# Optimization experiments

Hardware: AMD Instinct MI355X
Metric: run time of the kernel (lower is better)

## Reference

```python
import jax, jax.numpy as jnp
import numpy as np

BN_EPS = 1e-5

def _bn(h, gamma, beta):
    # training-mode BatchNorm1d over node dim, biased variance (as torch)
    m = jnp.mean(h, axis=0)
    v = jnp.var(h, axis=0)
    return (h - m) * jax.lax.rsqrt(v + BN_EPS) * gamma + beta

def _gin(x, edge_index, W, b, n_nodes):
    # PyG GINConv (eps=0): h = Linear(x + sum_{j in N(i)} x_j)
    src, dst = edge_index[0], edge_index[1]
    agg = jax.ops.segment_sum(x[src], dst, num_segments=n_nodes)
    return (x + agg) @ W + b

def setup_inputs() -> dict:
    key = jax.random.key(0)
    ks = jax.random.split(key, 16)
    N, E, D, H, G = 50000, 800000, 128, 256, 64
    x = jax.random.normal(ks[0], (N, D), dtype=jnp.float32)
    edge_index = jax.random.randint(ks[1], (2, E), 0, N, dtype=jnp.int64)
    batch = jnp.sort(jax.random.randint(ks[2], (N,), 0, G, dtype=jnp.int64))
    s = 0.05
    return {
        "x": x, "edge_index": edge_index, "batch": batch, "num_graphs": G,
        "W1": jax.random.normal(ks[3], (D, H), jnp.float32) * s,
        "b1": jnp.zeros((H,), jnp.float32),
        "W2": jax.random.normal(ks[4], (H, H), jnp.float32) * s,
        "b2": jnp.zeros((H,), jnp.float32),
        "W3": jax.random.normal(ks[5], (H, H), jnp.float32) * s,
        "b3": jnp.zeros((H,), jnp.float32),
        "g1": jnp.ones((H,), jnp.float32), "be1": jnp.zeros((H,), jnp.float32),
        "g2": jnp.ones((H,), jnp.float32), "be2": jnp.zeros((H,), jnp.float32),
        "g3": jnp.ones((H,), jnp.float32), "be3": jnp.zeros((H,), jnp.float32),
        "fcW1": jax.random.normal(ks[6], (H, H), jnp.float32) * s,
        "fcb1": jnp.zeros((H,), jnp.float32),
        "fcW2": jax.random.normal(ks[7], (H, 1), jnp.float32) * s,
        "fcb2": jnp.zeros((1,), jnp.float32),
    }

def reference(x, edge_index, batch, num_graphs, W1, b1, W2, b2, W3, b3,
              g1, be1, g2, be2, g3, be3, fcW1, fcb1, fcW2, fcb2):
    n_nodes = x.shape[0]
    # dropout treated as identity (eval / deterministic)
    x1 = jax.nn.relu(_bn(_gin(x, edge_index, W1, b1, n_nodes), g1, be1))
    x2 = jax.nn.relu(_bn(_gin(x1, edge_index, W2, b2, n_nodes), g2, be2)) + x1
    x3 = jax.nn.relu(_bn(_gin(x2, edge_index, W3, b3, n_nodes), g3, be3)) + x2
    # global mean pool over graphs
    sums = jax.ops.segment_sum(x3, batch, num_segments=num_graphs)
    cnt = jax.ops.segment_sum(jnp.ones((n_nodes,), x3.dtype), batch, num_segments=num_graphs)
    pooled = sums / jnp.maximum(cnt, 1.0)[:, None]
    h = jax.nn.relu(pooled @ fcW1 + fcb1)
    return h @ fcW2 + fcb2
```

## Files before the change

kernel.cpp:

```cpp
#include <hip/hip_runtime.h>
#include <hip/hip_bf16.h>
#include <stdint.h>

#define HDIM 256
#define NGRAPH 64

typedef short s16x8 __attribute__((ext_vector_type(8)));
typedef float f32x4 __attribute__((ext_vector_type(4)));

__device__ __forceinline__ float bf2f(unsigned short u){
    union { unsigned int i; float f; } x; x.i = ((unsigned int)u) << 16; return x.f;
}
__device__ __forceinline__ unsigned short f2bf(float f){
    union { float f; unsigned int i; } x; x.f = f;
    unsigned int r = x.i + 0x7fffu + ((x.i >> 16) & 1u);
    return (unsigned short)(r >> 16);
}
__device__ __forceinline__ float ldf(const void* p, int i, int f32){
    return f32 ? ((const float*)p)[i] : bf2f(((const unsigned short*)p)[i]);
}

__global__ void detect_kernel(const unsigned short* __restrict__ x,
                              const int* __restrict__ ei, const int* __restrict__ batch,
                              int E, int N, int* __restrict__ flags){
    if (threadIdx.x == 0 && blockIdx.x == 0){
        int c = 0;
        for (int i = 0; i < 128; i++){
            unsigned e = (x[2 * i] >> 7) & 0xFFu;
            if (e >= 100u && e <= 140u) c++;
        }
        flags[0] = (c < 96) ? 1 : 0;
        int z = (ei[2*E - 1] == 0) && (ei[2*E - 3] == 0) && (ei[2*E - 5] == 0) && (ei[2*E - 7] == 0);
        flags[1] = z ? 1 : 0;
        flags[2] = (batch[N - 1] == 0) ? 1 : 0;
    }
}

__global__ void zero_kernel(int* __restrict__ p, int n){
    int i = blockIdx.x * 256 + threadIdx.x;
    if (i < n) p[i] = 0;
}

__global__ void cvt_kernel(const void* __restrict__ src, unsigned short* __restrict__ dst,
                           int n8, const int* __restrict__ flags){
    int i = blockIdx.x * 256 + threadIdx.x;
    if (i >= n8) return;
    int base = i * 8;
    int f32 = flags[0];
    unsigned short o[8];
    if (f32){
        const float* s = (const float*)src + base;
        float4 a = *(const float4*)s;
        float4 b = *(const float4*)(s + 4);
        o[0]=f2bf(a.x); o[1]=f2bf(a.y); o[2]=f2bf(a.z); o[3]=f2bf(a.w);
        o[4]=f2bf(b.x); o[5]=f2bf(b.y); o[6]=f2bf(b.z); o[7]=f2bf(b.w);
    } else {
        *(uint4*)o = *(const uint4*)((const unsigned short*)src + base);
    }
    *(uint4*)&dst[base] = *(uint4*)o;
}

__global__ void hist_kernel(const int* __restrict__ ei, int E, int N,
                            const int* __restrict__ flags, int* __restrict__ deg){
    int e = blockIdx.x * 256 + threadIdx.x;
    if (e < E){
        int is64 = flags[1];
        int d = is64 ? ei[2 * E + 2 * e] : ei[E + e];
        if ((unsigned)d < (unsigned)N) atomicAdd(&deg[d], 1);
    }
}

__global__ void scan1_kernel(const int* __restrict__ deg, int N,
                             int* __restrict__ incl, int* __restrict__ bsums){
    __shared__ int sm[256];
    int t = threadIdx.x;
    int i = blockIdx.x * 256 + t;
    int v = (i < N) ? deg[i] : 0;
    sm[t] = v; __syncthreads();
    for (int off = 1; off < 256; off <<= 1){
        int tv = (t >= off) ? sm[t - off] : 0;
        __syncthreads();
        sm[t] += tv;
        __syncthreads();
    }
    if (i < N) incl[i] = sm[t];
    if (t == 255) bsums[blockIdx.x] = sm[255];
}

__global__ void scan23_kernel(const int* __restrict__ deg, int N, int E, int nb,
                              const int* __restrict__ bsums, int* __restrict__ rowptr){
    __shared__ int sm[256];
    int t = threadIdx.x;
    int bid = blockIdx.x;
    sm[t] = (t < nb && t < bid) ? bsums[t] : 0;
    __syncthreads();
    for (int s = 128; s > 0; s >>= 1){
        if (t < s) sm[t] += sm[t + s];
        __syncthreads();
    }
    int prefix = sm[0];
    int i = bid * 256 + t;
    if (i < N) rowptr[i] = rowptr[i] - deg[i] + prefix;
    if (i == 0) rowptr[N] = E;
}

__global__ void fill_kernel(const int* __restrict__ ei, int E, int N,
                            const int* __restrict__ flags,
                            const int* __restrict__ rowptr, int* __restrict__ fillc,
                            int* __restrict__ csr){
    int e = blockIdx.x * 256 + threadIdx.x;
    if (e < E){
        int is64 = flags[1];
        int d = is64 ? ei[2 * E + 2 * e] : ei[E + e];
        int s = is64 ? ei[2 * e]         : ei[e];
        if ((unsigned)d < (unsigned)N){
            int p = atomicAdd(&fillc[d], 1);
            csr[rowptr[d] + p] = s;
        }
    }
}

__global__ void transpose3_kernel(const void* __restrict__ W1, unsigned short* __restrict__ Wt1,
                                  const void* __restrict__ W2, unsigned short* __restrict__ Wt2,
                                  const void* __restrict__ W3, unsigned short* __restrict__ Wt3,
                                  const int* __restrict__ flags){
    int f32 = flags[0];
    int bid = blockIdx.x;
    const void* W; unsigned short* Wt; int K, base;
    if (bid < 128)      { W = W1; Wt = Wt1; K = 128; base = bid; }
    else if (bid < 384) { W = W2; Wt = Wt2; K = 256; base = bid - 128; }
    else                { W = W3; Wt = Wt3; K = 256; base = bid - 384; }
    int idx = base * 256 + threadIdx.x;
    int n = idx / K, k = idx - n * K;
    Wt[idx] = f2bf(ldf(W, k * 256 + n, f32));
}

template<int C>
__global__ __launch_bounds__(256) void agg_vec(const unsigned short* __restrict__ feat, int ldi,
                                               const int* __restrict__ rowptr, const int* __restrict__ csr,
                                               unsigned short* __restrict__ Y, int ldo, int N){
    constexpr int L   = C / 8;
    constexpr int NPB = 256 / L;
    int node = blockIdx.x * NPB + threadIdx.x / L;
    int lane = threadIdx.x & (L - 1);
    if (node >= N) return;
    int c0 = lane * 8;
    const unsigned short* base = feat + c0;

    unsigned short t0[8];
    *(uint4*)t0 = *(const uint4*)&feat[(size_t)node * ldi + c0];
    float acc[8];
    #pragma unroll
    for (int j = 0; j < 8; j++) acc[j] = bf2f(t0[j]);

    int lo = rowptr[node], hi = rowptr[node + 1];
    int e = lo;
    for (; e + 3 < hi; e += 4){
        int s0 = csr[e], s1 = csr[e + 1], s2 = csr[e + 2], s3 = csr[e + 3];
        unsigned short ta[8], tb[8], tc[8], td[8];
        *(uint4*)ta = *(const uint4*)&base[(size_t)s0 * ldi];
        *(uint4*)tb = *(const uint4*)&base[(size_t)s1 * ldi];
        *(uint4*)tc = *(const uint4*)&base[(size_t)s2 * ldi];
        *(uint4*)td = *(const uint4*)&base[(size_t)s3 * ldi];
        #pragma unroll
        for (int j = 0; j < 8; j++)
            acc[j] += (bf2f(ta[j]) + bf2f(tb[j])) + (bf2f(tc[j]) + bf2f(td[j]));
    }
    for (; e < hi; e++){
        int s0 = csr[e];
        unsigned short ta[8];
        *(uint4*)ta = *(const uint4*)&base[(size_t)s0 * ldi];
        #pragma unroll
        for (int j = 0; j < 8; j++) acc[j] += bf2f(ta[j]);
    }
    unsigned short o[8];
    #pragma unroll
    for (int j = 0; j < 8; j++) o[j] = f2bf(acc[j]);
    *(uint4*)&Y[(size_t)node * ldo + c0] = *(uint4*)o;
}

__global__ __launch_bounds__(256) void gemm_tile(
    unsigned short* __restrict__ AC, int K,
    const unsigned short* __restrict__ Bt, const void* __restrict__ bias,
    int M, const int* __restrict__ flags,
    float* __restrict__ S, float* __restrict__ Q)
{
    __shared__ __align__(16) unsigned short As[64 * 40];
    __shared__ __align__(16) unsigned short Bs[256 * 40];
    __shared__ float sS[256], sQ[256];
    const int tid  = threadIdx.x;
    const int wave = tid >> 6, lane = tid & 63;
    const int quad = lane >> 4, l16 = lane & 15;
    const int m0   = blockIdx.x * 64;
    const int wn   = wave * 64;
    const bool full = (m0 + 64 <= M);
    const int f32  = flags[0];

    sS[tid] = 0.f; sQ[tid] = 0.f;

    const f32x4 zero4 = {0.f, 0.f, 0.f, 0.f};
    f32x4 acc[4][4];
    #pragma unroll
    for (int i = 0; i < 4; i++)
        #pragma unroll
        for (int j = 0; j < 4; j++) acc[i][j] = zero4;

    for (int kc = 0; kc < K; kc += 32){
        {
            int r = tid >> 2, cc = (tid & 3) * 8;
            int gr = m0 + r;
            uint4 va; va.x = va.y = va.z = va.w = 0u;
            if (full || gr < M) va = *(const uint4*)&AC[(size_t)gr * HDIM + kc + cc];
            *(uint4*)&As[r * 40 + cc] = va;
        }
        #pragma unroll
        for (int j = 0; j < 4; j++){
            int c = tid + j * 256;
            int n = c >> 2, cc = (c & 3) * 8;
            *(uint4*)&Bs[n * 40 + cc] = *(const uint4*)&Bt[(size_t)n * K + kc + cc];
        }
        __syncthreads();
        s16x8 af[4], bfr[4];
        #pragma unroll
        for (int mt = 0; mt < 4; mt++)
            af[mt] = *(const s16x8*)&As[(mt * 16 + l16) * 40 + quad * 8];
        #pragma unroll
        for (int nt = 0; nt < 4; nt++)
            bfr[nt] = *(const s16x8*)&Bs[(wn + nt * 16 + l16) * 40 + quad * 8];
        #pragma unroll
        for (int mt = 0; mt < 4; mt++)
            #pragma unroll
            for (int nt = 0; nt < 4; nt++)
                acc[mt][nt] = __builtin_amdgcn_mfma_f32_16x16x32_bf16(af[mt], bfr[nt], acc[mt][nt], 0, 0, 0);
        __syncthreads();
    }
    #pragma unroll
    for (int nt = 0; nt < 4; nt++){
        int gc = wn + nt * 16 + l16;
        float bv = ldf(bias, gc, f32);
        float ps = 0.f, pq = 0.f;
        #pragma unroll
        for (int mt = 0; mt < 4; mt++){
            #pragma unroll
            for (int r = 0; r < 4; r++){
                int gr = m0 + mt * 16 + quad * 4 + r;
                if (full || gr < M){
                    float val = acc[mt][nt][r] + bv;
                    AC[(size_t)gr * HDIM + gc] = f2bf(val);
                    ps += val; pq += val * val;
                }
            }
        }
        atomicAdd(&sS[gc], ps);
        atomicAdd(&sQ[gc], pq);
    }
    __syncthreads();
    atomicAdd(&S[tid], sS[tid]);
    atomicAdd(&Q[tid], sQ[tid]);
}

__global__ void bnrelu_kernel(const unsigned short* __restrict__ Hin,
                              const float* __restrict__ S, const float* __restrict__ Q,
                              const void* __restrict__ g, const void* __restrict__ be,
                              float invM, const int* __restrict__ flags,
                              const unsigned short* __restrict__ res,
                              unsigned short* __restrict__ Out, int total16){
    __shared__ float sscale[256], sshift[256];
    int tid = threadIdx.x;
    {
        int f32 = flags[0];
        float m  = S[tid] * invM;
        float v  = Q[tid] * invM - m * m;
        float sc = ldf(g, tid, f32) * rsqrtf(v + 1e-5f);
        sscale[tid] = sc;
        sshift[tid] = ldf(be, tid, f32) - m * sc;
    }
    __syncthreads();
    int idx = blockIdx.x * 256 + tid;
    if (idx >= total16) return;
    #pragma unroll
    for (int h = 0; h < 2; h++){
        int base = idx * 16 + h * 8;
        int c = base & (HDIM - 1);
        unsigned short hv[8], rv[8], ov[8];
        *(uint4*)hv = *(const uint4*)&Hin[base];
        if (res) *(uint4*)rv = *(const uint4*)&res[base];
        #pragma unroll
        for (int j = 0; j < 8; j++){
            float v = bf2f(hv[j]) * sscale[c + j] + sshift[c + j];
            v = (v < 0.f) ? 0.f : v;
            if (res) v += bf2f(rv[j]);
            ov[j] = f2bf(v);
        }
        *(uint4*)&Out[base] = *(uint4*)ov;
    }
}

__global__ __launch_bounds__(256) void bnrelu_pool_kernel(
    const unsigned short* __restrict__ H, const unsigned short* __restrict__ res,
    const float* __restrict__ S, const float* __restrict__ Q,
    const void* __restrict__ g, const void* __restrict__ be,
    float invM, const int* __restrict__ flags,
    const int* __restrict__ batch, int N, float* __restrict__ sums)
{
    int r0 = blockIdx.x * 128;
    if (r0 >= N) return;
    int r1 = min(r0 + 128, N);
    int t = threadIdx.x;
    int f32 = flags[0];
    float m  = S[t] * invM;
    float v  = Q[t] * invM - m * m;
    float sc = ldf(g, t, f32) * rsqrtf(v + 1e-5f);
    float sh = ldf(be, t, f32) - m * sc;
    int stride = flags[2] ? 2 : 1;
    float acc = 0.f;
    int curg = batch[r0 * stride];
    for (int r = r0; r < r1; r++){
        int gg = batch[r * stride];
        if (gg != curg){
            atomicAdd(&sums[curg * HDIM + t], acc);
            acc = 0.f; curg = gg;
        }
        float hv = bf2f(H[(size_t)r * HDIM + t]) * sc + sh;
        hv = (hv < 0.f) ? 0.f : hv;
        hv += bf2f(res[(size_t)r * HDIM + t]);
        acc += hv;
    }
    atomicAdd(&sums[curg * HDIM + t], acc);
}

__global__ __launch_bounds__(256) void head_kernel(const float* __restrict__ sums,
                                                   const int* __restrict__ batch, int N,
                                                   const void* __restrict__ fcW1,
                                                   const void* __restrict__ fcb1,
                                                   const void* __restrict__ fcW2,
                                                   const void* __restrict__ fcb2,
                                                   void* __restrict__ out,
                                                   const int* __restrict__ flags){
    __shared__ float sp[256];
    __shared__ float red[256];
    __shared__ int scnt;
    int g = blockIdx.x, j = threadIdx.x;
    int f32 = flags[0];
    int stride = flags[2] ? 2 : 1;
    if (j == 0){
        int lo = 0, hi = N;
        while (lo < hi){ int mid = (lo + hi) >> 1; if (batch[mid * stride] < g) lo = mid + 1; else hi = mid; }
        int a = lo;
        lo = 0; hi = N;
        while (lo < hi){ int mid = (lo + hi) >> 1; if (batch[mid * stride] < g + 1) lo = mid + 1; else hi = mid; }
        scnt = lo - a;
    }
    __syncthreads();
    sp[j] = sums[g * HDIM + j] / (float)max(scnt, 1);
    __syncthreads();
    float acc = ldf(fcb1, j, f32);
    for (int k = 0; k < HDIM; k++) acc += sp[k] * ldf(fcW1, k * HDIM + j, f32);
    acc = (acc < 0.f) ? 0.f : acc;
    red[j] = acc * ldf(fcW2, j, f32);
    __syncthreads();
    for (int s = 128; s > 0; s >>= 1){
        if (j < s) red[j] += red[j + s];
        __syncthreads();
    }
    if (j == 0){
        float r = red[0] + ldf(fcb2, 0, f32);
        if (f32) ((float*)out)[g] = r;
        else     ((unsigned short*)out)[g] = f2bf(r);
    }
}

extern "C" void kernel_launch(void* const* d_in, const int* in_sizes, int n_in,
                              void* d_out, int out_size, void* d_ws, size_t ws_size,
                              hipStream_t stream)
{
    const unsigned short* x    = (const unsigned short*)d_in[0];
    const int*            ei   = (const int*)d_in[1];
    const int*            batch= (const int*)d_in[2];
    const void* W1   = d_in[4];
    const void* b1   = d_in[5];
    const void* W2   = d_in[6];
    const void* b2   = d_in[7];
    const void* W3   = d_in[8];
    const void* b3   = d_in[9];
    const void* g1   = d_in[10];
    const void* be1  = d_in[11];
    const void* g2   = d_in[12];
    const void* be2  = d_in[13];
    const void* g3   = d_in[14];
    const void* be3  = d_in[15];
    const void* fcW1 = d_in[16];
    const void* fcb1 = d_in[17];
    const void* fcW2 = d_in[18];
    const void* fcb2 = d_in[19];

    const int N = in_sizes[0] / 128;
    const int E = in_sizes[1] / 2;
    const int D = 128;

    char* p = (char*)d_ws;
    int*   deg     = (int*)p;   p += (size_t)N * 4;
    int*   fillc   = (int*)p;   p += (size_t)N * 4;
    float* stats   = (float*)p; p += 6 * 256 * 4;
    float* poolsum = (float*)p; p += NGRAPH * HDIM * 4;
    size_t zbytes  = (size_t)(p - (char*)d_ws);
    int*   flags   = (int*)p;   p += 16 * 4;
    int*   bsums   = (int*)p;   p += 256 * 4;
    int*   rowptr  = (int*)p;   p += ((size_t)N + 4) * 4;
    int*   csr     = (int*)p;   p += (size_t)E * 4;
    unsigned short* Wt1 = (unsigned short*)p; p += 256 * 128 * 2;
    unsigned short* Wt2 = (unsigned short*)p; p += 256 * 256 * 2;
    unsigned short* Wt3 = (unsigned short*)p; p += 256 * 256 * 2;
    unsigned short* B1  = (unsigned short*)p; p += (size_t)N * HDIM * 2;
    unsigned short* B2  = (unsigned short*)p; p += (size_t)N * HDIM * 2;
    unsigned short* Xc  = B1;

    float* S0 = stats + 0 * 256; float* Q0 = stats + 1 * 256;
    float* S1 = stats + 2 * 256; float* Q1 = stats + 3 * 256;
    float* S2 = stats + 4 * 256; float* Q2 = stats + 5 * 256;

    const int nbN = (N + 255) / 256;
    const int nbE = (E + 255) / 256;
    const int gM64  = (N + 63) / 64;
    const int gM128 = (N + 127) / 128;
    const float invM = 1.0f / (float)N;
    const int total16 = N * HDIM / 16;
    const int zn = (int)(zbytes / 4);
    const int nx8 = N * D / 8;

    detect_kernel<<<1, 64, 0, stream>>>(x, ei, batch, E, N, flags);
    zero_kernel<<<(zn + 255) / 256, 256, 0, stream>>>((int*)d_ws, zn);

    hist_kernel<<<nbE, 256, 0, stream>>>(ei, E, N, flags, deg);
    scan1_kernel<<<nbN, 256, 0, stream>>>(deg, N, rowptr, bsums);
    scan23_kernel<<<nbN, 256, 0, stream>>>(deg, N, E, nbN, bsums, rowptr);
    fill_kernel<<<nbE, 256, 0, stream>>>(ei, E, N, flags, rowptr, fillc, csr);

    transpose3_kernel<<<640, 256, 0, stream>>>(W1, Wt1, W2, Wt2, W3, Wt3, flags);
    cvt_kernel<<<(nx8 + 255) / 256, 256, 0, stream>>>(x, Xc, nx8, flags);

    agg_vec<128><<<(N + 15) / 16, 256, 0, stream>>>(Xc, D, rowptr, csr, B2, HDIM, N);
    gemm_tile<<<gM64, 256, 0, stream>>>(B2, 128, Wt1, b1, N, flags, S0, Q0);
    bnrelu_kernel<<<(total16 + 255) / 256, 256, 0, stream>>>(
        B2, S0, Q0, g1, be1, invM, flags, (const unsigned short*)nullptr, B1, total16);

    agg_vec<256><<<(N + 7) / 8, 256, 0, stream>>>(B1, HDIM, rowptr, csr, B2, HDIM, N);
    gemm_tile<<<gM64, 256, 0, stream>>>(B2, 256, Wt2, b2, N, flags, S1, Q1);
    bnrelu_kernel<<<(total16 + 255) / 256, 256, 0, stream>>>(
        B2, S1, Q1, g2, be2, invM, flags, B1, B1, total16);

    agg_vec<256><<<(N + 7) / 8, 256, 0, stream>>>(B1, HDIM, rowptr, csr, B2, HDIM, N);
    gemm_tile<<<gM64, 256, 0, stream>>>(B2, 256, Wt3, b3, N, flags, S2, Q2);
    bnrelu_pool_kernel<<<gM128, 256, 0, stream>>>(
        B2, B1, S2, Q2, g3, be3, invM, flags, batch, N, poolsum);

    head_kernel<<<NGRAPH, 256, 0, stream>>>(poolsum, batch, N, fcW1, fcb1, fcW2, fcb2, d_out, flags);

    (void)n_in; (void)out_size; (void)ws_size;
}
```

Before: 630.8 us.

## Fuse layer-1 BN+ReLU into aggregation, merge prep kernels, widen GEMM K-chunk

Layer-1 BatchNorm+ReLU now runs inside the layer-2 aggregation kernel on every gathered neighbour row, so x1 is never materialised. It is recomputed later in a dual-BN kernel that forms x2 = relu(bn2) + relu(bn1). The zero/detect and transpose/convert kernels are merged to cut launch count. The GEMM K-chunk grows from 32 to 64 to halve the sync barriers per tile. The trade-off is redundant BN arithmetic per edge in exchange for removing one full N×256 write+read pass, plus larger LDS use in the GEMM.

```diff
diff --git a/kernel.cpp b/kernel.cpp
--- a/kernel.cpp
+++ b/kernel.cpp
@@ -20,13 +20,16 @@
     return f32 ? ((const float*)p)[i] : bf2f(((const unsigned short*)p)[i]);
 }
 
-__global__ void detect_kernel(const unsigned short* __restrict__ x,
-                              const int* __restrict__ ei, const int* __restrict__ batch,
-                              int E, int N, int* __restrict__ flags){
-    if (threadIdx.x == 0 && blockIdx.x == 0){
+__global__ void zero_detect_kernel(int* __restrict__ p, int n,
+                                   const unsigned short* __restrict__ x,
+                                   const int* __restrict__ ei, const int* __restrict__ batch,
+                                   int E, int N, int* __restrict__ flags){
+    int i = blockIdx.x * 256 + threadIdx.x;
+    if (i < n) p[i] = 0;
+    if (i == 0){
         int c = 0;
-        for (int i = 0; i < 128; i++){
-            unsigned e = (x[2 * i] >> 7) & 0xFFu;
+        for (int k = 0; k < 128; k++){
+            unsigned e = (x[2 * k] >> 7) & 0xFFu;
             if (e >= 100u && e <= 140u) c++;
         }
         flags[0] = (c < 96) ? 1 : 0;
@@ -34,30 +37,6 @@
         flags[1] = z ? 1 : 0;
         flags[2] = (batch[N - 1] == 0) ? 1 : 0;
     }
-}
-
-__global__ void zero_kernel(int* __restrict__ p, int n){
-    int i = blockIdx.x * 256 + threadIdx.x;
-    if (i < n) p[i] = 0;
-}
-
-__global__ void cvt_kernel(const void* __restrict__ src, unsigned short* __restrict__ dst,
-                           int n8, const int* __restrict__ flags){
-    int i = blockIdx.x * 256 + threadIdx.x;
-    if (i >= n8) return;
-    int base = i * 8;
-    int f32 = flags[0];
-    unsigned short o[8];
-    if (f32){
-        const float* s = (const float*)src + base;
-        float4 a = *(const float4*)s;
-        float4 b = *(const float4*)(s + 4);
-        o[0]=f2bf(a.x); o[1]=f2bf(a.y); o[2]=f2bf(a.z); o[3]=f2bf(a.w);
-        o[4]=f2bf(b.x); o[5]=f2bf(b.y); o[6]=f2bf(b.z); o[7]=f2bf(b.w);
-    } else {
-        *(uint4*)o = *(const uint4*)((const unsigned short*)src + base);
-    }
-    *(uint4*)&dst[base] = *(uint4*)o;
 }
 
 __global__ void hist_kernel(const int* __restrict__ ei, int E, int N,
@@ -120,19 +99,37 @@
     }
 }
 
-__global__ void transpose3_kernel(const void* __restrict__ W1, unsigned short* __restrict__ Wt1,
-                                  const void* __restrict__ W2, unsigned short* __restrict__ Wt2,
-                                  const void* __restrict__ W3, unsigned short* __restrict__ Wt3,
-                                  const int* __restrict__ flags){
+__global__ void prep_kernel(const void* __restrict__ W1, unsigned short* __restrict__ Wt1,
+                            const void* __restrict__ W2, unsigned short* __restrict__ Wt2,
+                            const void* __restrict__ W3, unsigned short* __restrict__ Wt3,
+                            const void* __restrict__ x, unsigned short* __restrict__ Xc,
+                            int nx8, const int* __restrict__ flags){
+    int bid = blockIdx.x;
     int f32 = flags[0];
-    int bid = blockIdx.x;
-    const void* W; unsigned short* Wt; int K, base;
-    if (bid < 128)      { W = W1; Wt = Wt1; K = 128; base = bid; }
-    else if (bid < 384) { W = W2; Wt = Wt2; K = 256; base = bid - 128; }
-    else                { W = W3; Wt = Wt3; K = 256; base = bid - 384; }
-    int idx = base * 256 + threadIdx.x;
-    int n = idx / K, k = idx - n * K;
-    Wt[idx] = f2bf(ldf(W, k * 256 + n, f32));
+    if (bid < 640){
+        const void* W; unsigned short* Wt; int K, base;
+        if (bid < 128)      { W = W1; Wt = Wt1; K = 128; base = bid; }
+        else if (bid < 384) { W = W2; Wt = Wt2; K = 256; base = bid - 128; }
+        else                { W = W3; Wt = Wt3; K = 256; base = bid - 384; }
+        int idx = base * 256 + threadIdx.x;
+        int n = idx / K, k = idx - n * K;
+        Wt[idx] = f2bf(ldf(W, k * 256 + n, f32));
+    } else {
+        int i = (bid - 640) * 256 + threadIdx.x;
+        if (i >= nx8) return;
+        int base = i * 8;
+        unsigned short o[8];
+        if (f32){
+            const float* s = (const float*)x + base;
+            float4 a = *(const float4*)s;
+            float4 b = *(const float4*)(s + 4);
+            o[0]=f2bf(a.x); o[1]=f2bf(a.y); o[2]=f2bf(a.z); o[3]=f2bf(a.w);
+            o[4]=f2bf(b.x); o[5]=f2bf(b.y); o[6]=f2bf(b.z); o[7]=f2bf(b.w);
+        } else {
+            *(uint4*)o = *(const uint4*)((const unsigned short*)x + base);
+        }
+        *(uint4*)&Xc[base] = *(uint4*)o;
+    }
 }
 
 template<int C>
@@ -179,14 +176,76 @@
     *(uint4*)&Y[(size_t)node * ldo + c0] = *(uint4*)o;
 }
 
+__global__ __launch_bounds__(256) void agg_bn_vec(const unsigned short* __restrict__ H,
+                                                  const float* __restrict__ S, const float* __restrict__ Q,
+                                                  const void* __restrict__ g, const void* __restrict__ be,
+                                                  float invM, const int* __restrict__ flags,
+                                                  const int* __restrict__ rowptr, const int* __restrict__ csr,
+                                                  unsigned short* __restrict__ Y, int N){
+    constexpr int L = 32, NPB = 8;
+    int node = blockIdx.x * NPB + threadIdx.x / L;
+    int lane = threadIdx.x & (L - 1);
+    if (node >= N) return;
+    int c0 = lane * 8;
+    int f32 = flags[0];
+    float sc[8], sh[8];
+    #pragma unroll
+    for (int j = 0; j < 8; j++){
+        int col = c0 + j;
+        float m = S[col] * invM;
+        float v = Q[col] * invM - m * m;
+        float s = ldf(g, col, f32) * rsqrtf(v + 1e-5f);
+        sc[j] = s;
+        sh[j] = ldf(be, col, f32) - m * s;
+    }
+    const unsigned short* base = H + c0;
+
+    unsigned short t0[8];
+    *(uint4*)t0 = *(const uint4*)&base[(size_t)node * HDIM];
+    float acc[8];
+    #pragma unroll
+    for (int j = 0; j < 8; j++){
+        float v = bf2f(t0[j]) * sc[j] + sh[j];
+        acc[j] = (v < 0.f) ? 0.f : v;
+    }
+    int lo = rowptr[node], hi = rowptr[node + 1];
+    int e = lo;
+    for (; e + 1 < hi; e += 2){
+        int s0 = csr[e], s1 = csr[e + 1];
+        unsigned short ta[8], tb[8];
+        *(uint4*)ta = *(const uint4*)&base[(size_t)s0 * HDIM];
+        *(uint4*)tb = *(const uint4*)&base[(size_t)s1 * HDIM];
+        #pragma unroll
+        for (int j = 0; j < 8; j++){
+            float va = bf2f(ta[j]) * sc[j] + sh[j]; va = (va < 0.f) ? 0.f : va;
+            float vb = bf2f(tb[j]) * sc[j] + sh[j]; vb = (vb < 0.f) ? 0.f : vb;
+            acc[j] += va + vb;
+        }
+    }
+    if (e < hi){
+        int s0 = csr[e];
+        unsigned short ta[8];
+        *(uint4*)ta = *(const uint4*)&base[(size_t)s0 * HDIM];
+        #pragma unroll
+        for (int j = 0; j < 8; j++){
+            float va = bf2f(ta[j]) * sc[j] + sh[j]; va = (va < 0.f) ? 0.f : va;
+            acc[j] += va;
+        }
+    }
+    unsigned short o[8];
+    #pragma unroll
+    for (int j = 0; j < 8; j++) o[j] = f2bf(acc[j]);
+    *(uint4*)&Y[(size_t)node * HDIM + c0] = *(uint4*)o;
+}
+
 __global__ __launch_bounds__(256) void gemm_tile(
     unsigned short* __restrict__ AC, int K,
     const unsigned short* __restrict__ Bt, const void* __restrict__ bias,
     int M, const int* __restrict__ flags,
     float* __restrict__ S, float* __restrict__ Q)
 {
-    __shared__ __align__(16) unsigned short As[64 * 40];
-    __shared__ __align__(16) unsigned short Bs[256 * 40];
+    __shared__ __align__(16) unsigned short As[64 * 72];
+    __shared__ __align__(16) unsigned short Bs[256 * 72];
     __shared__ float sS[256], sQ[256];
     const int tid  = threadIdx.x;
     const int wave = tid >> 6, lane = tid & 63;
@@ -205,33 +264,38 @@
         #pragma unroll
         for (int j = 0; j < 4; j++) acc[i][j] = zero4;
 
-    for (int kc = 0; kc < K; kc += 32){
-        {
-            int r = tid >> 2, cc = (tid & 3) * 8;
+    for (int kc = 0; kc < K; kc += 64){
+        #pragma unroll
+        for (int j = 0; j < 2; j++){
+            int c = tid + j * 256;
+            int r = c >> 3, cc = (c & 7) * 8;
             int gr = m0 + r;
             uint4 va; va.x = va.y = va.z = va.w = 0u;
             if (full || gr < M) va = *(const uint4*)&AC[(size_t)gr * HDIM + kc + cc];
-            *(uint4*)&As[r * 40 + cc] = va;
-        }
-        #pragma unroll
-        for (int j = 0; j < 4; j++){
+            *(uint4*)&As[r * 72 + cc] = va;
+        }
+        #pragma unroll
+        for (int j = 0; j < 8; j++){
             int c = tid + j * 256;
-            int n = c >> 2, cc = (c & 3) * 8;
-            *(uint4*)&Bs[n * 40 + cc] = *(const uint4*)&Bt[(size_t)n * K + kc + cc];
+            int n = c >> 3, cc = (c & 7) * 8;
+            *(uint4*)&Bs[n * 72 + cc] = *(const uint4*)&Bt[(size_t)n * K + kc + cc];
         }
         __syncthreads();
-        s16x8 af[4], bfr[4];
-        #pragma unroll
-        for (int mt = 0; mt < 4; mt++)
-            af[mt] = *(const s16x8*)&As[(mt * 16 + l16) * 40 + quad * 8];
-        #pragma unroll
-        for (int nt = 0; nt < 4; nt++)
-            bfr[nt] = *(const s16x8*)&Bs[(wn + nt * 16 + l16) * 40 + quad * 8];
-        #pragma unroll
-        for (int mt = 0; mt < 4; mt++)
+        #pragma unroll
+        for (int kp = 0; kp < 64; kp += 32){
+            s16x8 af[4], bfr[4];
+            #pragma unroll
+            for (int mt = 0; mt < 4; mt++)
+                af[mt] = *(const s16x8*)&As[(mt * 16 + l16) * 72 + kp + quad * 8];
             #pragma unroll
             for (int nt = 0; nt < 4; nt++)
-                acc[mt][nt] = __builtin_amdgcn_mfma_f32_16x16x32_bf16(af[mt], bfr[nt], acc[mt][nt], 0, 0, 0);
+                bfr[nt] = *(const s16x8*)&Bs[(wn + nt * 16 + l16) * 72 + kp + quad * 8];
+            #pragma unroll
+            for (int mt = 0; mt < 4; mt++)
+                #pragma unroll
+                for (int nt = 0; nt < 4; nt++)
+                    acc[mt][nt] = __builtin_amdgcn_mfma_f32_16x16x32_bf16(af[mt], bfr[nt], acc[mt][nt], 0, 0, 0);
+        }
         __syncthreads();
     }
     #pragma unroll
@@ -259,21 +323,26 @@
     atomicAdd(&Q[tid], sQ[tid]);
 }
 
-__global__ void bnrelu_kernel(const unsigned short* __restrict__ Hin,
-                              const float* __restrict__ S, const float* __restrict__ Q,
-                              const void* __restrict__ g, const void* __restrict__ be,
-                              float invM, const int* __restrict__ flags,
-                              const unsigned short* __restrict__ res,
-                              unsigned short* __restrict__ Out, int total16){
-    __shared__ float sscale[256], sshift[256];
+__global__ void bnrelu2_kernel(const unsigned short* __restrict__ Hin,
+                               const float* __restrict__ Sc, const float* __restrict__ Qc,
+                               const void* __restrict__ gc_, const void* __restrict__ bec,
+                               const unsigned short* __restrict__ Hres,
+                               const float* __restrict__ Sp, const float* __restrict__ Qp,
+                               const void* __restrict__ gp, const void* __restrict__ bep,
+                               float invM, const int* __restrict__ flags,
+                               unsigned short* __restrict__ Out, int total16){
+    __shared__ float scA[256], shA[256], scB[256], shB[256];
     int tid = threadIdx.x;
     {
         int f32 = flags[0];
-        float m  = S[tid] * invM;
-        float v  = Q[tid] * invM - m * m;
-        float sc = ldf(g, tid, f32) * rsqrtf(v + 1e-5f);
-        sscale[tid] = sc;
-        sshift[tid] = ldf(be, tid, f32) - m * sc;
+        float m  = Sc[tid] * invM;
+        float v  = Qc[tid] * invM - m * m;
+        float s  = ldf(gc_, tid, f32) * rsqrtf(v + 1e-5f);
+        scA[tid] = s; shA[tid] = ldf(bec, tid, f32) - m * s;
+        m = Sp[tid] * invM;
+        v = Qp[tid] * invM - m * m;
+        s = ldf(gp, tid, f32) * rsqrtf(v + 1e-5f);
+        scB[tid] = s; shB[tid] = ldf(bep, tid, f32) - m * s;
     }
     __syncthreads();
     int idx = blockIdx.x * 256 + tid;
@@ -284,13 +353,14 @@
         int c = base & (HDIM - 1);
         unsigned short hv[8], rv[8], ov[8];
         *(uint4*)hv = *(const uint4*)&Hin[base];
-        if (res) *(uint4*)rv = *(const uint4*)&res[base];
+        *(uint4*)rv = *(const uint4*)&Hres[base];
         #pragma unroll
         for (int j = 0; j < 8; j++){
-            float v = bf2f(hv[j]) * sscale[c + j] + sshift[c + j];
+            float v = bf2f(hv[j]) * scA[c + j] + shA[c + j];
             v = (v < 0.f) ? 0.f : v;
-            if (res) v += bf2f(rv[j]);
-            ov[j] = f2bf(v);
+            float w = bf2f(rv[j]) * scB[c + j] + shB[c + j];
+            w = (w < 0.f) ? 0.f : w;
+            ov[j] = f2bf(v + w);
         }
         *(uint4*)&Out[base] = *(uint4*)ov;
     }
@@ -428,31 +498,28 @@
     const int zn = (int)(zbytes / 4);
     const int nx8 = N * D / 8;
 
-    detect_kernel<<<1, 64, 0, stream>>>(x, ei, batch, E, N, flags);
-    zero_kernel<<<(zn + 255) / 256, 256, 0, stream>>>((int*)d_ws, zn);
+    zero_detect_kernel<<<(zn + 255) / 256, 256, 0, stream>>>((int*)d_ws, zn, x, ei, batch, E, N, flags);
 
     hist_kernel<<<nbE, 256, 0, stream>>>(ei, E, N, flags, deg);
     scan1_kernel<<<nbN, 256, 0, stream>>>(deg, N, rowptr, bsums);
     scan23_kernel<<<nbN, 256, 0, stream>>>(deg, N, E, nbN, bsums, rowptr);
     fill_kernel<<<nbE, 256, 0, stream>>>(ei, E, N, flags, rowptr, fillc, csr);
 
-    transpose3_kernel<<<640, 256, 0, stream>>>(W1, Wt1, W2, Wt2, W3, Wt3, flags);
-    cvt_kernel<<<(nx8 + 255) / 256, 256, 0, stream>>>(x, Xc, nx8, flags);
+    prep_kernel<<<640 + (nx8 + 255) / 256, 256, 0, stream>>>(W1, Wt1, W2, Wt2, W3, Wt3, x, Xc, nx8, flags);
 
     agg_vec<128><<<(N + 15) / 16, 256, 0, stream>>>(Xc, D, rowptr, csr, B2, HDIM, N);
     gemm_tile<<<gM64, 256, 0, stream>>>(B2, 128, Wt1, b1, N, flags, S0, Q0);
-    bnrelu_kernel<<<(total16 + 255) / 256, 256, 0, stream>>>(
-        B2, S0, Q0, g1, be1, invM, flags, (const unsigned short*)nullptr, B1, total16);
-
-    agg_vec<256><<<(N + 7) / 8, 256, 0, stream>>>(B1, HDIM, rowptr, csr, B2, HDIM, N);
-    gemm_tile<<<gM64, 256, 0, stream>>>(B2, 256, Wt2, b2, N, flags, S1, Q1);
-    bnrelu_kernel<<<(total16 + 255) / 256, 256, 0, stream>>>(
-        B2, S1, Q1, g2, be2, invM, flags, B1, B1, total16);
-
-    agg_vec<256><<<(N + 7) / 8, 256, 0, stream>>>(B1, HDIM, rowptr, csr, B2, HDIM, N);
-    gemm_tile<<<gM64, 256, 0, stream>>>(B2, 256, Wt3, b3, N, flags, S2, Q2);
+
+    agg_bn_vec<<<(N + 7) / 8, 256, 0, stream>>>(B2, S0, Q0, g1, be1, invM, flags, rowptr, csr, B1, N);
+    gemm_tile<<<gM64, 256, 0, stream>>>(B1, 256, Wt2, b2, N, flags, S1, Q1);
+
+    bnrelu2_kernel<<<(total16 + 255) / 256, 256, 0, stream>>>(
+        B1, S1, Q1, g2, be2, B2, S0, Q0, g1, be1, invM, flags, B2, total16);
+
+    agg_vec<256><<<(N + 7) / 8, 256, 0, stream>>>(B2, HDIM, rowptr, csr, B1, HDIM, N);
+    gemm_tile<<<gM64, 256, 0, stream>>>(B1, 256, Wt3, b3, N, flags, S2, Q2);
     bnrelu_pool_kernel<<<gM128, 256, 0, stream>>>(
-        B2, B1, S2, Q2, g3, be3, invM, flags, batch, N, poolsum);
+        B1, B2, S2, Q2, g3, be3, invM, flags, batch, N, poolsum);
 
     head_kernel<<<NGRAPH, 256, 0, stream>>>(poolsum, batch, N, fcW1, fcb1, fcW2, fcb2, d_out, flags);
 
```

Result: slower. 670.5 us (+6.3%).
